# Performance work log

Measured on AMD Instinct MI355X. Metric: run time of the kernel, lower is better.

The kernel has to match this reference:

```python
import jax, jax.numpy as jnp
import numpy as np

B, S, H = 32, 2048, 1024


def setup_inputs() -> dict:
    key = jax.random.key(0)
    k1, k2, k3, k4, k5, k6 = jax.random.split(key, 6)
    scale = 1.0 / np.sqrt(H)
    return {
        "query": jax.random.normal(k1, (B, 1, H), dtype=jnp.float32),
        "encoder_outputs": jax.random.normal(k2, (B, S, H), dtype=jnp.float32),
        "src_lengths": jax.random.randint(k3, (B,), 0, S, dtype=jnp.int64),
        "W_h": jax.random.normal(k4, (H, H), dtype=jnp.float32) * scale,
        "W_s": jax.random.normal(k5, (H, H), dtype=jnp.float32) * scale,
        "v": jax.random.normal(k6, (H,), dtype=jnp.float32) * scale,
    }


def reference(query, encoder_outputs, src_lengths, W_h, W_s, v):
    # score(h_i, s) = v^T tanh(W_h h_i + W_s s)
    proj_h = jnp.einsum("bsh,hd->bsd", encoder_outputs, W_h)   # (B,S,H)
    proj_s = jnp.einsum("bqh,hd->bqd", query, W_s)             # (B,1,H)
    scores = jnp.einsum("bsd,d->bs", jnp.tanh(proj_h + proj_s), v)  # (B,S)
    # sequence mask: True for valid positions
    mask = jnp.arange(encoder_outputs.shape[1])[None, :] < src_lengths[:, None]
    scores = jnp.where(mask, scores, -1e9)
    attn_weights = jax.nn.softmax(scores, axis=1)              # (B,S)
    attn_out = jnp.einsum("bs,bsh->bh", attn_weights, encoder_outputs)
    return attn_out[:, None, :]  # (B,1,H)
```

## Files before the change

### kernel.cpp

```cpp
#include <hip/hip_runtime.h>
#include <hip/hip_bf16.h>
#include <stdint.h>

#define NB 32
#define NS 2048
#define NH 1024

typedef __attribute__((ext_vector_type(8))) unsigned short ushort8v;
typedef __attribute__((ext_vector_type(4))) unsigned short ushort4v;
typedef __attribute__((ext_vector_type(8))) __bf16 bf16x8;
typedef __attribute__((ext_vector_type(4))) float floatx4;

__device__ __forceinline__ unsigned short f2bf(float f) {
    union { float f; unsigned int u; } x; x.f = f;
    unsigned int r = x.u + 0x7fffu + ((x.u >> 16) & 1u);
    return (unsigned short)(r >> 16);
}
__device__ __forceinline__ float bf2f(unsigned short u) {
    union { unsigned int u; float f; } x; x.u = ((unsigned int)u) << 16;
    return x.f;
}
__device__ __forceinline__ float tanh_fast(float x) {
    float e2 = __expf(2.0f * x);
    return 1.0f - 2.0f * __builtin_amdgcn_rcpf(e2 + 1.0f);
}
__device__ __forceinline__ void gload_lds16(const void* g, void* l) {
    __builtin_amdgcn_global_load_lds(
        (const __attribute__((address_space(1))) unsigned int*)g,
        (__attribute__((address_space(3))) unsigned int*)l, 16, 0, 0);
}

__global__ void conve_kernel(const float* __restrict__ E,
                             const int* __restrict__ lens,
                             unsigned short* __restrict__ Ebf)
{
    int r = blockIdx.x;
    int len = lens[r >> 11];
    if (len != 0 && (r & (NS - 1)) >= len) return;
    int t = threadIdx.x;
    float4 f = *(const float4*)(E + (size_t)r * NH + t * 4);
    ushort4v u;
    u[0] = f2bf(f.x); u[1] = f2bf(f.y); u[2] = f2bf(f.z); u[3] = f2bf(f.w);
    *(ushort4v*)(Ebf + (size_t)r * NH + t * 4) = u;
}

__global__ void convw_projs_kernel(const float* __restrict__ Wh,
                                   unsigned short* __restrict__ WhP,
                                   const float* __restrict__ q,
                                   const float* __restrict__ Ws,
                                   float* __restrict__ projs)
{
    int t = threadIdx.x;
    if (blockIdx.x < 128) {
        int kb = blockIdx.x;
        int n  = t * 4;
        int ni = n & 15, nh = n >> 4;
        for (int i = 0; i < 8; ++i) {
            int k = kb * 8 + i;
            float4 w = *(const float4*)(Wh + (size_t)k * NH + n);
            size_t base = (size_t)nh * 16384 + (size_t)(k >> 5) * 512 + (k & 31);
            WhP[base + (size_t)(ni + 0) * 32] = f2bf(w.x);
            WhP[base + (size_t)(ni + 1) * 32] = f2bf(w.y);
            WhP[base + (size_t)(ni + 2) * 32] = f2bf(w.z);
            WhP[base + (size_t)(ni + 3) * 32] = f2bf(w.w);
        }
        return;
    }
    int lb = blockIdx.x - 128;
    int b  = lb >> 2;
    int d0 = (lb & 3) * 256;
    int kg = t >> 6;
    int dc = t & 63;
    const float* qb = q + (size_t)b * NH;
    float4 acc = {0.f, 0.f, 0.f, 0.f};
    for (int k = kg * 256; k < kg * 256 + 256; ++k) {
        float qv = qb[k];
        float4 wv = *(const float4*)(Ws + (size_t)k * NH + d0 + dc * 4);
        acc.x += qv * wv.x; acc.y += qv * wv.y;
        acc.z += qv * wv.z; acc.w += qv * wv.w;
    }
    __shared__ float4 red[4][64];
    red[kg][dc] = acc;
    __syncthreads();
    if (t < 64) {
        float4 s = red[0][t];
        float4 s1 = red[1][t], s2 = red[2][t], s3 = red[3][t];
        s.x += s1.x + s2.x + s3.x; s.y += s1.y + s2.y + s3.y;
        s.z += s1.z + s2.z + s3.z; s.w += s1.w + s2.w + s3.w;
        *(float4*)(projs + (size_t)b * NH + d0 + t * 4) = s;
    }
}

__global__ __launch_bounds__(512) void scores_kernel(
    const unsigned short* __restrict__ Ebf, const unsigned short* __restrict__ WhP,
    const float* __restrict__ projs, const float* __restrict__ v,
    const int* __restrict__ lens, float* __restrict__ spart)
{
    __shared__ __align__(16) unsigned short Al[3][4096];
    __shared__ __align__(16) unsigned short Bl[3][8192];
    __shared__ float sc[4][128];

    const int tid  = threadIdx.x;
    const int wgid = blockIdx.x;
    const int x    = wgid & 7;
    const int i    = wgid >> 3;
    const int cb   = i & 3;
    const int rt   = (i >> 2) * 8 + x;
    const int brow = rt * 128;
    const int b    = brow >> 11;
    const int sloc = brow & (NS - 1);
    if (sloc >= lens[b]) return;

    const int wave = tid >> 6;
    const int lane = tid & 63;
    const int l15 = lane & 15;
    const int l16 = lane >> 4;
    const int wr = wave >> 2;
    const int wc = wave & 3;

    floatx4 acc[4][4];
    #pragma unroll
    for (int m = 0; m < 4; ++m)
        #pragma unroll
        for (int c = 0; c < 4; ++c) acc[m][c] = (floatx4){0.f, 0.f, 0.f, 0.f};

    const int ssw = ((lane & 3) ^ ((lane >> 3) & 3)) * 8;

    const unsigned short* Asrc = Ebf
        + (size_t)(brow + wave * 16 + (lane >> 2)) * NH + ssw;
    const unsigned short* Bsrc0 = WhP
        + (size_t)(cb * 16 + wave * 2) * 16384 + (lane >> 2) * 32 + ssw;
    const unsigned short* Bsrc1 = Bsrc0 + 16384;

    #define STAGE(buf, kc)                                                     \
    {                                                                          \
        gload_lds16(Asrc + (size_t)(kc) * 32, (void*)&Al[buf][wave * 512]);    \
        gload_lds16(Bsrc0 + (size_t)(kc) * 512, (void*)&Bl[buf][(wave * 2) * 512]); \
        gload_lds16(Bsrc1 + (size_t)(kc) * 512, (void*)&Bl[buf][(wave * 2 + 1) * 512]); \
    }

    const int aslot = (l16 ^ ((l15 >> 1) & 3)) * 8;
    const int bslot = aslot;

    #define COMPUTE(buf)                                                       \
    {                                                                          \
        bf16x8 a[4], bfr[4];                                                   \
        _Pragma("unroll")                                                      \
        for (int m = 0; m < 4; ++m)                                            \
            a[m] = __builtin_bit_cast(bf16x8, *(const ushort8v*)               \
                &Al[buf][(wr * 64 + m * 16 + l15) * 32 + aslot]);              \
        _Pragma("unroll")                                                      \
        for (int c = 0; c < 4; ++c)                                            \
            bfr[c] = __builtin_bit_cast(bf16x8, *(const ushort8v*)             \
                &Bl[buf][(wc * 4 + c) * 512 + l15 * 32 + bslot]);              \
        __builtin_amdgcn_s_setprio(1);                                         \
        _Pragma("unroll")                                                      \
        for (int m = 0; m < 4; ++m)                                            \
            _Pragma("unroll")                                                  \
            for (int c = 0; c < 4; ++c)                                        \
                acc[m][c] = __builtin_amdgcn_mfma_f32_16x16x32_bf16(           \
                    a[m], bfr[c], acc[m][c], 0, 0, 0);                         \
        __builtin_amdgcn_s_setprio(0);                                         \
    }

    STAGE(0, 0);

    for (int kc = 0; kc < 31; ++kc) {
        const int rbuf = kc % 3;
        const int sbuf = (kc + 1) % 3;
        STAGE(sbuf, kc + 1);
        asm volatile("s_waitcnt vmcnt(3)" ::: "memory");
        __builtin_amdgcn_sched_barrier(0);
        __builtin_amdgcn_s_barrier();
        COMPUTE(rbuf);
    }
    asm volatile("s_waitcnt vmcnt(0)" ::: "memory");
    __builtin_amdgcn_sched_barrier(0);
    __builtin_amdgcn_s_barrier();
    COMPUTE(31 % 3);
    #undef STAGE
    #undef COMPUTE

    float psv[4], vv[4];
    #pragma unroll
    for (int c = 0; c < 4; ++c) {
        int col = cb * 256 + wc * 64 + c * 16 + l15;
        psv[c] = projs[(size_t)b * NH + col];
        vv[c]  = v[col];
    }
    #pragma unroll
    for (int m = 0; m < 4; ++m) {
        float sp[4] = {0.f, 0.f, 0.f, 0.f};
        #pragma unroll
        for (int c = 0; c < 4; ++c)
            #pragma unroll
            for (int i2 = 0; i2 < 4; ++i2)
                sp[i2] += tanh_fast(acc[m][c][i2] + psv[c]) * vv[c];
        #pragma unroll
        for (int i2 = 0; i2 < 4; ++i2) {
            float s = sp[i2];
            s += __shfl_xor(s, 1);
            s += __shfl_xor(s, 2);
            s += __shfl_xor(s, 4);
            s += __shfl_xor(s, 8);
            if (l15 == 0) sc[wc][wr * 64 + m * 16 + l16 * 4 + i2] = s;
        }
    }
    __syncthreads();
    if (tid < 128) {
        float s = sc[0][tid] + sc[1][tid] + sc[2][tid] + sc[3][tid];
        spart[(size_t)cb * (NB * NS) + brow + tid] = s;
    }
}

__global__ void softmax_kernel(const float* __restrict__ spart,
                               const int* __restrict__ lens,
                               float* __restrict__ wts)
{
    int b = blockIdx.x, tid = threadIdx.x;
    int len = lens[b];
    float loc[8];
    float mx = -3e38f;
    #pragma unroll
    for (int i = 0; i < 8; ++i) {
        int s = tid + i * 256;
        float val = -1e9f;
        if (s < len) {
            val = 0.f;
            #pragma unroll
            for (int c = 0; c < 4; ++c)
                val += spart[(size_t)c * (NB * NS) + (size_t)b * NS + s];
        }
        loc[i] = val;
        mx = fmaxf(mx, val);
    }
    #pragma unroll
    for (int m = 32; m >= 1; m >>= 1) mx = fmaxf(mx, __shfl_xor(mx, m));
    __shared__ float red[4], red2[4];
    int w = tid >> 6;
    if ((tid & 63) == 0) red[w] = mx;
    __syncthreads();
    mx = fmaxf(fmaxf(red[0], red[1]), fmaxf(red[2], red[3]));
    float sum = 0.f;
    #pragma unroll
    for (int i = 0; i < 8; ++i) { loc[i] = expf(loc[i] - mx); sum += loc[i]; }
    #pragma unroll
    for (int m = 32; m >= 1; m >>= 1) sum += __shfl_xor(sum, m);
    if ((tid & 63) == 0) red2[w] = sum;
    __syncthreads();
    sum = red2[0] + red2[1] + red2[2] + red2[3];
    float inv = 1.f / sum;
    #pragma unroll
    for (int i = 0; i < 8; ++i)
        wts[(size_t)b * NS + tid + i * 256] = loc[i] * inv;
}

__global__ void attnout1_kernel(const unsigned short* __restrict__ Ebf,
                                const float* __restrict__ wts,
                                const int* __restrict__ lens,
                                float* __restrict__ part)
{
    int b  = blockIdx.x;
    int ch = blockIdx.y;
    int s0 = ch * 128;
    int t  = threadIdx.x;
    int len = lens[b];
    float* po = part + ((size_t)ch * NB + b) * NH;
    if (len > 0 && s0 >= len) {
        *(float4*)(po + t * 4) = (float4){0.f, 0.f, 0.f, 0.f};
        return;
    }
    __shared__ float wsh[128];
    if (t < 128) wsh[t] = wts[(size_t)b * NS + s0 + t];
    __syncthreads();
    int h0 = t * 4;
    const unsigned short* Eb = Ebf + ((size_t)b * NS + s0) * NH + h0;
    float4 acc = {0.f, 0.f, 0.f, 0.f};
    for (int s = 0; s < 128; ++s) {
        float w = wsh[s];
        ushort4v e = *(const ushort4v*)(Eb + (size_t)s * NH);
        acc.x += w * bf2f(e[0]); acc.y += w * bf2f(e[1]);
        acc.z += w * bf2f(e[2]); acc.w += w * bf2f(e[3]);
    }
    *(float4*)(po + h0) = acc;
}

__global__ void attnout2_kernel(const float* __restrict__ part,
                                float* __restrict__ out)
{
    int b = blockIdx.x, t = threadIdx.x;
    float4 acc = {0.f, 0.f, 0.f, 0.f};
    #pragma unroll
    for (int c = 0; c < 16; ++c) {
        float4 p = *(const float4*)(part + ((size_t)c * NB + b) * NH + t * 4);
        acc.x += p.x; acc.y += p.y; acc.z += p.z; acc.w += p.w;
    }
    *(float4*)(out + (size_t)b * NH + t * 4) = acc;
}

extern "C" void kernel_launch(void* const* d_in, const int* in_sizes, int n_in,
                              void* d_out, int out_size, void* d_ws, size_t ws_size,
                              hipStream_t stream)
{
    const float* q    = (const float*)d_in[0];
    const float* E    = (const float*)d_in[1];
    const int*   lens = (const int*)d_in[2];
    const float* Wh   = (const float*)d_in[3];
    const float* Ws   = (const float*)d_in[4];
    const float* v    = (const float*)d_in[5];
    float* out = (float*)d_out;

    float* ws     = (float*)d_ws;
    float* projs  = ws;
    float* spart  = projs + 32 * 1024;
    float* wts    = spart + 4 * NB * NS;
    float* part   = wts + NB * NS;
    unsigned short* WhP = (unsigned short*)(part + 16 * NB * NH);
    unsigned short* Ebf = WhP + 1024 * 1024;

    conve_kernel      <<<NB * NS, 256, 0, stream>>>(E, lens, Ebf);
    convw_projs_kernel<<<256, 256, 0, stream>>>(Wh, WhP, q, Ws, projs);
    scores_kernel     <<<2048, 512, 0, stream>>>(Ebf, WhP, projs, v, lens, spart);
    softmax_kernel    <<<NB, 256, 0, stream>>>(spart, lens, wts);
    attnout1_kernel   <<<dim3(NB, 16), 256, 0, stream>>>(Ebf, wts, lens, part);
    attnout2_kernel   <<<NB, 256, 0, stream>>>(part, out);
}
```

Before: 166.8 us.

## Fuse prep kernels, fold softmax into attention-out, remap score tile order

Merges the E conversion and W/proj_s prep kernels into a single launch, and removes the separate softmax kernel. Each attnout1 block now recomputes the per-batch max and sum from the partial scores before building its own weights. The scores kernel's block-to-tile mapping is also changed so that consecutive XCD-interleaved blocks cover the four column blocks of the same row tile. This saves two launches and a weights round trip, at the cost of redundant softmax reductions in each of the 16 chunk blocks per batch.

```diff
diff --git a/kernel.cpp b/kernel.cpp
--- a/kernel.cpp
+++ b/kernel.cpp
@@ -30,29 +30,29 @@
         (__attribute__((address_space(3))) unsigned int*)l, 16, 0, 0);
 }
 
-__global__ void conve_kernel(const float* __restrict__ E,
-                             const int* __restrict__ lens,
-                             unsigned short* __restrict__ Ebf)
-{
-    int r = blockIdx.x;
-    int len = lens[r >> 11];
-    if (len != 0 && (r & (NS - 1)) >= len) return;
-    int t = threadIdx.x;
-    float4 f = *(const float4*)(E + (size_t)r * NH + t * 4);
-    ushort4v u;
-    u[0] = f2bf(f.x); u[1] = f2bf(f.y); u[2] = f2bf(f.z); u[3] = f2bf(f.w);
-    *(ushort4v*)(Ebf + (size_t)r * NH + t * 4) = u;
-}
-
-__global__ void convw_projs_kernel(const float* __restrict__ Wh,
-                                   unsigned short* __restrict__ WhP,
-                                   const float* __restrict__ q,
-                                   const float* __restrict__ Ws,
-                                   float* __restrict__ projs)
-{
-    int t = threadIdx.x;
-    if (blockIdx.x < 128) {
-        int kb = blockIdx.x;
+__global__ void prep_kernel(const float* __restrict__ E,
+                            const int* __restrict__ lens,
+                            unsigned short* __restrict__ Ebf,
+                            const float* __restrict__ Wh,
+                            unsigned short* __restrict__ WhP,
+                            const float* __restrict__ q,
+                            const float* __restrict__ Ws,
+                            float* __restrict__ projs)
+{
+    const int bid = blockIdx.x;
+    const int t   = threadIdx.x;
+    if (bid >= 256) {
+        int r = bid - 256;
+        int len = lens[r >> 11];
+        if (len != 0 && (r & (NS - 1)) >= len) return;
+        float4 f = *(const float4*)(E + (size_t)r * NH + t * 4);
+        ushort4v u;
+        u[0] = f2bf(f.x); u[1] = f2bf(f.y); u[2] = f2bf(f.z); u[3] = f2bf(f.w);
+        *(ushort4v*)(Ebf + (size_t)r * NH + t * 4) = u;
+        return;
+    }
+    if (bid < 128) {
+        int kb = bid;
         int n  = t * 4;
         int ni = n & 15, nh = n >> 4;
         for (int i = 0; i < 8; ++i) {
@@ -66,28 +66,30 @@
         }
         return;
     }
-    int lb = blockIdx.x - 128;
-    int b  = lb >> 2;
-    int d0 = (lb & 3) * 256;
-    int kg = t >> 6;
-    int dc = t & 63;
-    const float* qb = q + (size_t)b * NH;
-    float4 acc = {0.f, 0.f, 0.f, 0.f};
-    for (int k = kg * 256; k < kg * 256 + 256; ++k) {
-        float qv = qb[k];
-        float4 wv = *(const float4*)(Ws + (size_t)k * NH + d0 + dc * 4);
-        acc.x += qv * wv.x; acc.y += qv * wv.y;
-        acc.z += qv * wv.z; acc.w += qv * wv.w;
-    }
-    __shared__ float4 red[4][64];
-    red[kg][dc] = acc;
-    __syncthreads();
-    if (t < 64) {
-        float4 s = red[0][t];
-        float4 s1 = red[1][t], s2 = red[2][t], s3 = red[3][t];
-        s.x += s1.x + s2.x + s3.x; s.y += s1.y + s2.y + s3.y;
-        s.z += s1.z + s2.z + s3.z; s.w += s1.w + s2.w + s3.w;
-        *(float4*)(projs + (size_t)b * NH + d0 + t * 4) = s;
+    {
+        int lb = bid - 128;
+        int b  = lb >> 2;
+        int d0 = (lb & 3) * 256;
+        int kg = t >> 6;
+        int dc = t & 63;
+        const float* qb = q + (size_t)b * NH;
+        float4 acc = {0.f, 0.f, 0.f, 0.f};
+        for (int k = kg * 256; k < kg * 256 + 256; ++k) {
+            float qv = qb[k];
+            float4 wv = *(const float4*)(Ws + (size_t)k * NH + d0 + dc * 4);
+            acc.x += qv * wv.x; acc.y += qv * wv.y;
+            acc.z += qv * wv.z; acc.w += qv * wv.w;
+        }
+        __shared__ float4 red[4][64];
+        red[kg][dc] = acc;
+        __syncthreads();
+        if (t < 64) {
+            float4 s = red[0][t];
+            float4 s1 = red[1][t], s2 = red[2][t], s3 = red[3][t];
+            s.x += s1.x + s2.x + s3.x; s.y += s1.y + s2.y + s3.y;
+            s.z += s1.z + s2.z + s3.z; s.w += s1.w + s2.w + s3.w;
+            *(float4*)(projs + (size_t)b * NH + d0 + t * 4) = s;
+        }
     }
 }
 
@@ -102,11 +104,9 @@
 
     const int tid  = threadIdx.x;
     const int wgid = blockIdx.x;
-    const int x    = wgid & 7;
-    const int i    = wgid >> 3;
-    const int cb   = i & 3;
-    const int rt   = (i >> 2) * 8 + x;
-    const int brow = rt * 128;
+    const int vid  = (wgid & 7) * 256 + (wgid >> 3);
+    const int brow = (vid >> 2) * 128;
+    const int cb   = vid & 3;
     const int b    = brow >> 11;
     const int sloc = brow & (NS - 1);
     if (sloc >= lens[b]) return;
@@ -213,50 +213,8 @@
     }
 }
 
-__global__ void softmax_kernel(const float* __restrict__ spart,
-                               const int* __restrict__ lens,
-                               float* __restrict__ wts)
-{
-    int b = blockIdx.x, tid = threadIdx.x;
-    int len = lens[b];
-    float loc[8];
-    float mx = -3e38f;
-    #pragma unroll
-    for (int i = 0; i < 8; ++i) {
-        int s = tid + i * 256;
-        float val = -1e9f;
-        if (s < len) {
-            val = 0.f;
-            #pragma unroll
-            for (int c = 0; c < 4; ++c)
-                val += spart[(size_t)c * (NB * NS) + (size_t)b * NS + s];
-        }
-        loc[i] = val;
-        mx = fmaxf(mx, val);
-    }
-    #pragma unroll
-    for (int m = 32; m >= 1; m >>= 1) mx = fmaxf(mx, __shfl_xor(mx, m));
-    __shared__ float red[4], red2[4];
-    int w = tid >> 6;
-    if ((tid & 63) == 0) red[w] = mx;
-    __syncthreads();
-    mx = fmaxf(fmaxf(red[0], red[1]), fmaxf(red[2], red[3]));
-    float sum = 0.f;
-    #pragma unroll
-    for (int i = 0; i < 8; ++i) { loc[i] = expf(loc[i] - mx); sum += loc[i]; }
-    #pragma unroll
-    for (int m = 32; m >= 1; m >>= 1) sum += __shfl_xor(sum, m);
-    if ((tid & 63) == 0) red2[w] = sum;
-    __syncthreads();
-    sum = red2[0] + red2[1] + red2[2] + red2[3];
-    float inv = 1.f / sum;
-    #pragma unroll
-    for (int i = 0; i < 8; ++i)
-        wts[(size_t)b * NS + tid + i * 256] = loc[i] * inv;
-}
-
 __global__ void attnout1_kernel(const unsigned short* __restrict__ Ebf,
-                                const float* __restrict__ wts,
+                                const float* __restrict__ spart,
                                 const int* __restrict__ lens,
                                 float* __restrict__ part)
 {
@@ -270,17 +228,57 @@
         *(float4*)(po + t * 4) = (float4){0.f, 0.f, 0.f, 0.f};
         return;
     }
+    const float* p0 = spart + (size_t)b * NS;
+    float loc[8];
+    float mx = -3e38f;
+    #pragma unroll
+    for (int i = 0; i < 8; ++i) {
+        int s = t + i * 256;
+        float val = -1e9f;
+        if (s < len) {
+            val = 0.f;
+            #pragma unroll
+            for (int c = 0; c < 4; ++c) val += p0[(size_t)c * (NB * NS) + s];
+        }
+        loc[i] = val;
+        mx = fmaxf(mx, val);
+    }
+    #pragma unroll
+    for (int m = 32; m >= 1; m >>= 1) mx = fmaxf(mx, __shfl_xor(mx, m));
+    __shared__ float red[4], red2[4];
     __shared__ float wsh[128];
-    if (t < 128) wsh[t] = wts[(size_t)b * NS + s0 + t];
+    int w = t >> 6;
+    if ((t & 63) == 0) red[w] = mx;
+    __syncthreads();
+    mx = fmaxf(fmaxf(red[0], red[1]), fmaxf(red[2], red[3]));
+    float sum = 0.f;
+    #pragma unroll
+    for (int i = 0; i < 8; ++i) sum += expf(loc[i] - mx);
+    #pragma unroll
+    for (int m = 32; m >= 1; m >>= 1) sum += __shfl_xor(sum, m);
+    if ((t & 63) == 0) red2[w] = sum;
+    __syncthreads();
+    sum = red2[0] + red2[1] + red2[2] + red2[3];
+    float inv = 1.f / sum;
+    if (t < 128) {
+        int s = s0 + t;
+        float val = -1e9f;
+        if (s < len) {
+            val = 0.f;
+            #pragma unroll
+            for (int c = 0; c < 4; ++c) val += p0[(size_t)c * (NB * NS) + s];
+        }
+        wsh[t] = expf(val - mx) * inv;
+    }
     __syncthreads();
     int h0 = t * 4;
     const unsigned short* Eb = Ebf + ((size_t)b * NS + s0) * NH + h0;
     float4 acc = {0.f, 0.f, 0.f, 0.f};
     for (int s = 0; s < 128; ++s) {
-        float w = wsh[s];
+        float wv = wsh[s];
         ushort4v e = *(const ushort4v*)(Eb + (size_t)s * NH);
-        acc.x += w * bf2f(e[0]); acc.y += w * bf2f(e[1]);
-        acc.z += w * bf2f(e[2]); acc.w += w * bf2f(e[3]);
+        acc.x += wv * bf2f(e[0]); acc.y += wv * bf2f(e[1]);
+        acc.z += wv * bf2f(e[2]); acc.w += wv * bf2f(e[3]);
     }
     *(float4*)(po + h0) = acc;
 }
@@ -313,15 +311,12 @@
     float* ws     = (float*)d_ws;
     float* projs  = ws;
     float* spart  = projs + 32 * 1024;
-    float* wts    = spart + 4 * NB * NS;
-    float* part   = wts + NB * NS;
+    float* part   = spart + 4 * NB * NS;
     unsigned short* WhP = (unsigned short*)(part + 16 * NB * NH);
     unsigned short* Ebf = WhP + 1024 * 1024;
 
-    conve_kernel      <<<NB * NS, 256, 0, stream>>>(E, lens, Ebf);
-    convw_projs_kernel<<<256, 256, 0, stream>>>(Wh, WhP, q, Ws, projs);
-    scores_kernel     <<<2048, 512, 0, stream>>>(Ebf, WhP, projs, v, lens, spart);
-    softmax_kernel    <<<NB, 256, 0, stream>>>(spart, lens, wts);
-    attnout1_kernel   <<<dim3(NB, 16), 256, 0, stream>>>(Ebf, wts, lens, part);
-    attnout2_kernel   <<<NB, 256, 0, stream>>>(part, out);
-}
+    prep_kernel    <<<256 + NB * NS, 256, 0, stream>>>(E, lens, Ebf, Wh, WhP, q, Ws, projs);
+    scores_kernel  <<<2048, 512, 0, stream>>>(Ebf, WhP, projs, v, lens, spart);
+    attnout1_kernel<<<dim3(NB, 16), 256, 0, stream>>>(Ebf, spart, lens, part);
+    attnout2_kernel<<<NB, 256, 0, stream>>>(part, out);
+}
```

Result: faster. 148.6 us (median of 3 runs) (-10.9%).
